# Optimization experiments

Hardware: AMD Instinct MI355X
Metric: run time of the kernel (lower is better)

Reference implementation:

```python
import jax, jax.numpy as jnp
import numpy as np

ALPHA = 0.2          # LeakyReLU negative slope
NEG_BIG = -9e15      # mask value from original code


def setup_inputs() -> dict:
    key = jax.random.key(0)
    k1, k2, k3, k4 = jax.random.split(key, 4)
    B, N, F_in, F_out = 16, 1024, 256, 256
    x = jax.random.normal(k1, (B, N, F_in), dtype=jnp.float32)
    adj = jax.random.randint(k2, (B, N, N), 0, 2, dtype=jnp.int32)
    # xavier-uniform-like scales
    W = jax.random.normal(k3, (F_in, F_out), dtype=jnp.float32) * np.sqrt(2.0 / (F_in + F_out))
    a = jax.random.normal(k4, (2 * F_out, 1), dtype=jnp.float32) * np.sqrt(2.0 / (2 * F_out + 1))
    return {"x": x, "adj": adj, "W": W, "a": a}


def reference(x, adj, W, a):
    # x: [B,N,Fin], adj: [B,N,N] (int mask), W: [Fin,Fout], a: [2*Fout,1]
    F_out = a.shape[0] // 2
    h = jnp.einsum("bni,io->bno", x, W)            # [B,N,Fout]
    # Decompose a into left/right halves: e_ij = lrelu(a_l.h_i + a_r.h_j)
    a_l = a[:F_out, 0]                               # [Fout]
    a_r = a[F_out:, 0]                               # [Fout]
    el = h @ a_l                                     # [B,N] score contribution of target i
    er = h @ a_r                                     # [B,N] score contribution of source j
    e = jax.nn.leaky_relu(el[:, :, None] + er[:, None, :], ALPHA)  # [B,N,N]
    e = jnp.where(adj > 0, e, NEG_BIG)
    attn = jax.nn.softmax(e, axis=-1)                # masked softmax over neighbors j
    # weighted sum of neighbor features; concat with n_heads=1 is identity
    return jnp.einsum("bij,bjo->bio", attn, h)       # [B,N,Fout]
```

## Files before the change

kernel.cpp:

```cpp
#include <hip/hip_runtime.h>
#include <stdint.h>

#define ALPHA 0.2f
#define NEG_BIG -9000000000000000.0f
#define L2E 1.4426950408889634f

typedef __attribute__((ext_vector_type(8))) short bf16x8;
typedef __attribute__((ext_vector_type(8))) unsigned short u16x8;
typedef __attribute__((ext_vector_type(4))) float f32x4;

__device__ __forceinline__ unsigned short f2bf(float f) {
    unsigned int u = __float_as_uint(f);
    u += 0x7fffu + ((u >> 16) & 1u);
    return (unsigned short)(u >> 16);
}

__device__ __forceinline__ void gload_lds16(const void* g, void* l) {
    __builtin_amdgcn_global_load_lds(
        (const __attribute__((address_space(1))) unsigned int*)g,
        (__attribute__((address_space(3))) unsigned int*)l, 16, 0, 0);
}

__global__ void wt_wa_kernel(const float* __restrict__ W,
                             const float* __restrict__ a,
                             unsigned short* __restrict__ Wtbf,
                             float* __restrict__ wa) {
    const int t = threadIdx.x;
    if (blockIdx.x < 256) {
        const int o = blockIdx.x;
        Wtbf[o * 256 + t] = f2bf(W[t * 256 + o]);
    } else {
        float sl = 0.f, sr = 0.f;
        const float* wr = W + t * 256;
        for (int o = 0; o < 256; ++o) {
            const float wv = wr[o];
            sl += wv * a[o];
            sr += wv * a[256 + o];
        }
        wa[t] = sl;
        wa[256 + t] = sr;
    }
}

__global__ __launch_bounds__(256) void eler2x_kernel(
    const float* __restrict__ x, const float* __restrict__ wa,
    float* __restrict__ el, float* __restrict__ er,
    unsigned short* __restrict__ xbf)
{
    const int w = threadIdx.x >> 6, l = threadIdx.x & 63;
    const int r = blockIdx.x * 4 + w;
    const float4 xv = *(const float4*)(x + (size_t)r * 256 + l * 4);
    const float4 al = *(const float4*)(wa + l * 4);
    const float4 ar = *(const float4*)(wa + 256 + l * 4);

    ushort4 xb;
    xb.x = f2bf(xv.x); xb.y = f2bf(xv.y); xb.z = f2bf(xv.z); xb.w = f2bf(xv.w);
    *(ushort4*)(xbf + (size_t)r * 256 + l * 4) = xb;

    float sl = xv.x * al.x + xv.y * al.y + xv.z * al.z + xv.w * al.w;
    float sr = xv.x * ar.x + xv.y * ar.y + xv.z * ar.z + xv.w * ar.w;
#pragma unroll
    for (int off = 32; off >= 1; off >>= 1) {
        sl += __shfl_xor(sl, off);
        sr += __shfl_xor(sr, off);
    }
    if (l == 0) { el[r] = sl * L2E; er[r] = sr * L2E; }
}

__global__ __launch_bounds__(256) void gemm_h(
    const unsigned short* __restrict__ A,
    const unsigned short* __restrict__ Bt,
    unsigned short* __restrict__ C)
{
    __shared__ __align__(16) unsigned short As[2 * 64 * 64];
    __shared__ __align__(16) unsigned short Bs[2 * 128 * 64];

    const int tid = threadIdx.x;
    const int w = tid >> 6, l = tid & 63;
    const int q = l >> 4, ml = l & 15;
    const int wm = (w >> 1) * 32;
    const int wn = (w & 1) * 64;
    const int m0 = blockIdx.y * 64;
    const int n0 = blockIdx.x * 128;

    f32x4 acc[2][4];
#pragma unroll
    for (int i = 0; i < 2; ++i)
#pragma unroll
        for (int j = 0; j < 4; ++j) {
            f32x4 z = {0.f, 0.f, 0.f, 0.f};
            acc[i][j] = z;
        }

#define GSTAGE(BI, K0) do {                                                   \
    _Pragma("unroll")                                                         \
    for (int c_ = 0; c_ < 2; ++c_) {                                          \
        const int cb_ = c_ * 256 + (w << 6);                                  \
        const int p_ = cb_ + l;                                               \
        const int r_ = p_ >> 3;                                               \
        const int cc_ = (p_ & 7) ^ (r_ & 7);                                  \
        gload_lds16(A + (size_t)(m0 + r_) * 256 + (K0) + cc_ * 8,             \
                    As + (BI) * 4096 + cb_ * 8);                              \
    }                                                                         \
    _Pragma("unroll")                                                         \
    for (int c_ = 0; c_ < 4; ++c_) {                                          \
        const int cb_ = c_ * 256 + (w << 6);                                  \
        const int p_ = cb_ + l;                                               \
        const int r_ = p_ >> 3;                                               \
        const int cc_ = (p_ & 7) ^ (r_ & 7);                                  \
        gload_lds16(Bt + (size_t)(n0 + r_) * 256 + (K0) + cc_ * 8,            \
                    Bs + (BI) * 8192 + cb_ * 8);                              \
    } } while (0)

    GSTAGE(0, 0);

    for (int s = 0; s < 4; ++s) {
        const int cur = s & 1;
        if (s + 1 < 4) {
            GSTAGE((s + 1) & 1, (s + 1) * 64);
            asm volatile("s_waitcnt vmcnt(6) lgkmcnt(0)" ::: "memory");
        } else {
            asm volatile("s_waitcnt vmcnt(0) lgkmcnt(0)" ::: "memory");
        }
        __builtin_amdgcn_s_barrier();
        __builtin_amdgcn_sched_barrier(0);

        const unsigned short* Ab = As + cur * 4096;
        const unsigned short* Bb = Bs + cur * 8192;
        bf16x8 aF[2][2], bF[2][4];
#pragma unroll
        for (int ks = 0; ks < 2; ++ks) {
#pragma unroll
            for (int mt = 0; mt < 2; ++mt) {
                const int mm = wm + mt * 16 + ml;
                aF[ks][mt] = *(const bf16x8*)(Ab + (mm * 8 + ((ks * 4 + q) ^ (mm & 7))) * 8);
            }
#pragma unroll
            for (int nt = 0; nt < 4; ++nt) {
                const int nn = wn + nt * 16 + ml;
                bF[ks][nt] = *(const bf16x8*)(Bb + (nn * 8 + ((ks * 4 + q) ^ (nn & 7))) * 8);
            }
        }
#pragma unroll
        for (int ks = 0; ks < 2; ++ks)
            for (int mt = 0; mt < 2; ++mt)
                for (int nt = 0; nt < 4; ++nt)
                    acc[mt][nt] = __builtin_amdgcn_mfma_f32_16x16x32_bf16(
                        aF[ks][mt], bF[ks][nt], acc[mt][nt], 0, 0, 0);

        asm volatile("s_waitcnt lgkmcnt(0)" ::: "memory");
        __builtin_amdgcn_s_barrier();
    }
#undef GSTAGE

    for (int mt = 0; mt < 2; ++mt)
        for (int nt = 0; nt < 4; ++nt) {
            const int gn = n0 + wn + nt * 16 + ml;
            for (int r = 0; r < 4; ++r) {
                const int gm = m0 + wm + mt * 16 + q * 4 + r;
                C[(size_t)gm * 16384 + gn] = f2bf(acc[mt][nt][r]);
            }
        }
}

__global__ __launch_bounds__(512) void maskpv_kernel(
    const int* __restrict__ adj,
    const float* __restrict__ el2,
    const float* __restrict__ er2,
    const unsigned short* __restrict__ hT,
    float* __restrict__ out)
{
    __shared__ float er_s[1024];
    __shared__ float c_s[32];
    __shared__ __align__(16) unsigned short Hs[2 * 256 * 64];
    __shared__ __align__(16) unsigned short Ps[2 * 32 * 72];

    const int tid = threadIdx.x;
    const int w = tid >> 6, l = tid & 63;
    const int q = l >> 4, ml = l & 15;
    const int wm = (w >> 2) * 16;
    const int wn = (w & 3) * 64;

    const int bid = blockIdx.x;
    const int slot = bid >> 3;
    const int b = ((bid & 7) << 1) | (slot >> 5);
    const int i0 = (slot & 31) * 32;

    const int ib = tid >> 4;
    const int js = (tid & 15) * 4;
    const int rg = (b << 10) + i0 + ib;
    const float el2i = el2[rg];

    const unsigned short* hb = hT + (size_t)b * 1024;

#define STAGE(BI, T) do {                                                     \
    const int jb_ = (T) * 64;                                                 \
    _Pragma("unroll")                                                         \
    for (int c_ = 0; c_ < 4; ++c_) {                                          \
        const int cb_ = c_ * 512 + tid;                                       \
        const int r_ = cb_ >> 3;                                              \
        const int cc_ = (cb_ & 7) ^ (r_ & 7);                                 \
        gload_lds16(hb + (size_t)r_ * 16384 + jb_ + cc_ * 8,                  \
                    Hs + (BI) * 16384 + (cb_ << 3));                          \
    } } while (0)

    STAGE(0, 0);

    *(float2*)(er_s + tid * 2) = *(const float2*)(er2 + (b << 10) + tid * 2);
    asm volatile("s_waitcnt lgkmcnt(0)" ::: "memory");
    __builtin_amdgcn_s_barrier();

    unsigned mw0 = 0, mw1 = 0;
    float m1 = -3.0e38f;
    const int* arow = adj + (size_t)rg * 1024 + js;
#pragma unroll
    for (int k = 0; k < 16; ++k) {
        const int4 av = *(const int4*)(arow + k * 64);
        const float4 erv = *(const float4*)(er_s + k * 64 + js);
        float e0 = el2i + erv.x; e0 = fmaxf(e0, ALPHA * e0);
        float e1 = el2i + erv.y; e1 = fmaxf(e1, ALPHA * e1);
        float e2 = el2i + erv.z; e2 = fmaxf(e2, ALPHA * e2);
        float e3 = el2i + erv.w; e3 = fmaxf(e3, ALPHA * e3);
        const unsigned bits = (av.x > 0 ? 1u : 0u) | (av.y > 0 ? 2u : 0u) |
                              (av.z > 0 ? 4u : 0u) | (av.w > 0 ? 8u : 0u);
        e0 = av.x > 0 ? e0 : -3.0e38f;
        e1 = av.y > 0 ? e1 : -3.0e38f;
        e2 = av.z > 0 ? e2 : -3.0e38f;
        e3 = av.w > 0 ? e3 : -3.0e38f;
        m1 = fmaxf(m1, fmaxf(fmaxf(e0, e1), fmaxf(e2, e3)));
        if (k < 8) mw0 |= bits << (k * 4); else mw1 |= bits << ((k - 8) * 4);
    }
#pragma unroll
    for (int off = 1; off <= 8; off <<= 1) m1 = fmaxf(m1, __shfl_xor(m1, off));

    float s0 = 0.f, s1 = 0.f, s2 = 0.f, s3 = 0.f;
#pragma unroll
    for (int k = 0; k < 16; ++k) {
        const float4 erv = *(const float4*)(er_s + k * 64 + js);
        const unsigned mv = ((k < 8) ? (mw0 >> (k * 4)) : (mw1 >> ((k - 8) * 4))) & 0xFu;
        float e0 = el2i + erv.x; e0 = fmaxf(e0, ALPHA * e0);
        float e1 = el2i + erv.y; e1 = fmaxf(e1, ALPHA * e1);
        float e2 = el2i + erv.z; e2 = fmaxf(e2, ALPHA * e2);
        float e3 = el2i + erv.w; e3 = fmaxf(e3, ALPHA * e3);
        s0 += (mv & 1u) ? exp2f(e0 - m1) : 0.f;
        s1 += (mv & 2u) ? exp2f(e1 - m1) : 0.f;
        s2 += (mv & 4u) ? exp2f(e2 - m1) : 0.f;
        s3 += (mv & 8u) ? exp2f(e3 - m1) : 0.f;
    }
    float ssum = (s0 + s1) + (s2 + s3);
#pragma unroll
    for (int off = 1; off <= 8; off <<= 1) ssum += __shfl_xor(ssum, off);
    if ((tid & 15) == 0) c_s[ib] = m1 + log2f(ssum);
    asm volatile("s_waitcnt lgkmcnt(0)" ::: "memory");
    __builtin_amdgcn_s_barrier();
    const float c2i = c_s[ib];

    f32x4 acc[4];
#pragma unroll
    for (int j = 0; j < 4; ++j) {
        f32x4 z = {0.f, 0.f, 0.f, 0.f};
        acc[j] = z;
    }

#define BUILDR(BI, T) do {                                                    \
    const float4 ev_ = *(const float4*)(er_s + (T) * 64 + js);                \
    const unsigned mv_ =                                                      \
        (((T) < 8) ? (mw0 >> ((T) * 4)) : (mw1 >> (((T) - 8) * 4))) & 0xFu;   \
    float e0_ = el2i + ev_.x; e0_ = fmaxf(e0_, ALPHA * e0_);                  \
    float e1_ = el2i + ev_.y; e1_ = fmaxf(e1_, ALPHA * e1_);                  \
    float e2_ = el2i + ev_.z; e2_ = fmaxf(e2_, ALPHA * e2_);                  \
    float e3_ = el2i + ev_.w; e3_ = fmaxf(e3_, ALPHA * e3_);                  \
    ushort4 pv_;                                                              \
    pv_.x = (mv_ & 1u) ? f2bf(exp2f(e0_ - c2i)) : (unsigned short)0;          \
    pv_.y = (mv_ & 2u) ? f2bf(exp2f(e1_ - c2i)) : (unsigned short)0;          \
    pv_.z = (mv_ & 4u) ? f2bf(exp2f(e2_ - c2i)) : (unsigned short)0;          \
    pv_.w = (mv_ & 8u) ? f2bf(exp2f(e3_ - c2i)) : (unsigned short)0;          \
    *(ushort4*)(Ps + (BI) * 2304 + ib * 72 + js) = pv_;                       \
    } while (0)

#define COMPUTE(BI) do {                                                      \
    bf16x8 aF_[2], bF_[2][4];                                                 \
    _Pragma("unroll")                                                         \
    for (int ks_ = 0; ks_ < 2; ++ks_)                                         \
        aF_[ks_] = *(const bf16x8*)(Ps + (BI) * 2304 +                        \
                                    (wm + ml) * 72 + ks_ * 32 + q * 8);       \
    _Pragma("unroll")                                                         \
    for (int ks_ = 0; ks_ < 2; ++ks_)                                         \
        _Pragma("unroll")                                                     \
        for (int nt_ = 0; nt_ < 4; ++nt_) {                                   \
            const int oc_ = wn + nt_ * 16 + ml;                               \
            const int sl_ = (ks_ * 4 + q) ^ (oc_ & 7);                        \
            bF_[ks_][nt_] = *(const bf16x8*)(Hs + (BI) * 16384 +              \
                                             oc_ * 64 + sl_ * 8);             \
        }                                                                     \
    _Pragma("unroll")                                                         \
    for (int ks_ = 0; ks_ < 2; ++ks_)                                         \
        _Pragma("unroll")                                                     \
        for (int nt_ = 0; nt_ < 4; ++nt_)                                     \
            acc[nt_] = __builtin_amdgcn_mfma_f32_16x16x32_bf16(               \
                aF_[ks_], bF_[ks_][nt_], acc[nt_], 0, 0, 0);                  \
    } while (0)

#pragma unroll
    for (int t = 0; t < 16; ++t) {
        const int cur = t & 1;
        if (t + 1 < 16) STAGE((t + 1) & 1, t + 1);
        BUILDR(cur, t);
        if (t + 1 < 16)
            asm volatile("s_waitcnt vmcnt(4) lgkmcnt(0)" ::: "memory");
        else
            asm volatile("s_waitcnt vmcnt(0) lgkmcnt(0)" ::: "memory");
        __builtin_amdgcn_s_barrier();
        __builtin_amdgcn_sched_barrier(0);
        COMPUTE(cur);
        asm volatile("s_waitcnt lgkmcnt(0)" ::: "memory");
        __builtin_amdgcn_s_barrier();
    }

#undef STAGE
#undef BUILDR
#undef COMPUTE

    float* ob = out + (size_t)b * 262144;
#pragma unroll
    for (int nt = 0; nt < 4; ++nt) {
        const int gn = wn + nt * 16 + ml;
#pragma unroll
        for (int r = 0; r < 4; ++r) {
            const int gm = i0 + wm + q * 4 + r;
            ob[(size_t)gm * 256 + gn] = acc[nt][r];
        }
    }
}

extern "C" void kernel_launch(void* const* d_in, const int* in_sizes, int n_in,
                              void* d_out, int out_size, void* d_ws, size_t ws_size,
                              hipStream_t stream) {
    const float* x   = (const float*)d_in[0];
    const int*   adj = (const int*)d_in[1];
    const float* W   = (const float*)d_in[2];
    const float* a   = (const float*)d_in[3];
    float* out = (float*)d_out;

    char* ws = (char*)d_ws;
    unsigned short* Wtbf  = (unsigned short*)(ws);
    float* wa             = (float*)(ws + 131072);
    unsigned short* xbf   = (unsigned short*)(ws + 133120);
    unsigned short* h_T   = (unsigned short*)(ws + 8521728);
    float* el             = (float*)(ws + 16910336);
    float* er             = (float*)(ws + 16975872);

    wt_wa_kernel<<<dim3(257), dim3(256), 0, stream>>>(W, a, Wtbf, wa);

    eler2x_kernel<<<dim3(4096), dim3(256), 0, stream>>>(x, wa, el, er, xbf);

    gemm_h<<<dim3(128, 4), dim3(256), 0, stream>>>(Wtbf, xbf, h_T);

    maskpv_kernel<<<dim3(512), dim3(512), 0, stream>>>(adj, el, er, h_T, out);
}
```

Before: 153.5 us.

## Fuse softmax statistics into PV loop with deferred row normalization

Drops the two prepass loops over the adjacency row (row max, then sum of exps). Scores are now exponentiated in the main tiled loop without subtracting a row max. The row sum is accumulated from the same bf16-rounded probabilities fed to the MFMA, and the output is divided by that sum at the end. Adjacency loads are now prefetched one tile ahead inside the pipelined loop, which removes a full serial pass of loads and exps before the matrix work. The cost is numerical safety: skipping max subtraction can overflow for large scores, and a row with no neighbours would divide by zero.

Result: slower. 157.8 us (+2.8%).

```diff
diff --git a/kernel.cpp b/kernel.cpp
--- a/kernel.cpp
+++ b/kernel.cpp
@@ -171,7 +171,7 @@
     float* __restrict__ out)
 {
     __shared__ float er_s[1024];
-    __shared__ float c_s[32];
+    __shared__ float s_s[32];
     __shared__ __align__(16) unsigned short Hs[2 * 256 * 64];
     __shared__ __align__(16) unsigned short Ps[2 * 32 * 72];
 
@@ -207,53 +207,12 @@
     STAGE(0, 0);
 
     *(float2*)(er_s + tid * 2) = *(const float2*)(er2 + (b << 10) + tid * 2);
+
+    const int* arow = adj + (size_t)rg * 1024 + js;
+    int4 a_cur = *(const int4*)(arow);
+
     asm volatile("s_waitcnt lgkmcnt(0)" ::: "memory");
     __builtin_amdgcn_s_barrier();
-
-    unsigned mw0 = 0, mw1 = 0;
-    float m1 = -3.0e38f;
-    const int* arow = adj + (size_t)rg * 1024 + js;
-#pragma unroll
-    for (int k = 0; k < 16; ++k) {
-        const int4 av = *(const int4*)(arow + k * 64);
-        const float4 erv = *(const float4*)(er_s + k * 64 + js);
-        float e0 = el2i + erv.x; e0 = fmaxf(e0, ALPHA * e0);
-        float e1 = el2i + erv.y; e1 = fmaxf(e1, ALPHA * e1);
-        float e2 = el2i + erv.z; e2 = fmaxf(e2, ALPHA * e2);
-        float e3 = el2i + erv.w; e3 = fmaxf(e3, ALPHA * e3);
-        const unsigned bits = (av.x > 0 ? 1u : 0u) | (av.y > 0 ? 2u : 0u) |
-                              (av.z > 0 ? 4u : 0u) | (av.w > 0 ? 8u : 0u);
-        e0 = av.x > 0 ? e0 : -3.0e38f;
-        e1 = av.y > 0 ? e1 : -3.0e38f;
-        e2 = av.z > 0 ? e2 : -3.0e38f;
-        e3 = av.w > 0 ? e3 : -3.0e38f;
-        m1 = fmaxf(m1, fmaxf(fmaxf(e0, e1), fmaxf(e2, e3)));
-        if (k < 8) mw0 |= bits << (k * 4); else mw1 |= bits << ((k - 8) * 4);
-    }
-#pragma unroll
-    for (int off = 1; off <= 8; off <<= 1) m1 = fmaxf(m1, __shfl_xor(m1, off));
-
-    float s0 = 0.f, s1 = 0.f, s2 = 0.f, s3 = 0.f;
-#pragma unroll
-    for (int k = 0; k < 16; ++k) {
-        const float4 erv = *(const float4*)(er_s + k * 64 + js);
-        const unsigned mv = ((k < 8) ? (mw0 >> (k * 4)) : (mw1 >> ((k - 8) * 4))) & 0xFu;
-        float e0 = el2i + erv.x; e0 = fmaxf(e0, ALPHA * e0);
-        float e1 = el2i + erv.y; e1 = fmaxf(e1, ALPHA * e1);
-        float e2 = el2i + erv.z; e2 = fmaxf(e2, ALPHA * e2);
-        float e3 = el2i + erv.w; e3 = fmaxf(e3, ALPHA * e3);
-        s0 += (mv & 1u) ? exp2f(e0 - m1) : 0.f;
-        s1 += (mv & 2u) ? exp2f(e1 - m1) : 0.f;
-        s2 += (mv & 4u) ? exp2f(e2 - m1) : 0.f;
-        s3 += (mv & 8u) ? exp2f(e3 - m1) : 0.f;
-    }
-    float ssum = (s0 + s1) + (s2 + s3);
-#pragma unroll
-    for (int off = 1; off <= 8; off <<= 1) ssum += __shfl_xor(ssum, off);
-    if ((tid & 15) == 0) c_s[ib] = m1 + log2f(ssum);
-    asm volatile("s_waitcnt lgkmcnt(0)" ::: "memory");
-    __builtin_amdgcn_s_barrier();
-    const float c2i = c_s[ib];
 
     f32x4 acc[4];
 #pragma unroll
@@ -261,20 +220,23 @@
         f32x4 z = {0.f, 0.f, 0.f, 0.f};
         acc[j] = z;
     }
+    float s0 = 0.f, s1 = 0.f, s2 = 0.f, s3 = 0.f;
 
 #define BUILDR(BI, T) do {                                                    \
     const float4 ev_ = *(const float4*)(er_s + (T) * 64 + js);                \
-    const unsigned mv_ =                                                      \
-        (((T) < 8) ? (mw0 >> ((T) * 4)) : (mw1 >> (((T) - 8) * 4))) & 0xFu;   \
     float e0_ = el2i + ev_.x; e0_ = fmaxf(e0_, ALPHA * e0_);                  \
     float e1_ = el2i + ev_.y; e1_ = fmaxf(e1_, ALPHA * e1_);                  \
     float e2_ = el2i + ev_.z; e2_ = fmaxf(e2_, ALPHA * e2_);                  \
     float e3_ = el2i + ev_.w; e3_ = fmaxf(e3_, ALPHA * e3_);                  \
     ushort4 pv_;                                                              \
-    pv_.x = (mv_ & 1u) ? f2bf(exp2f(e0_ - c2i)) : (unsigned short)0;          \
-    pv_.y = (mv_ & 2u) ? f2bf(exp2f(e1_ - c2i)) : (unsigned short)0;          \
-    pv_.z = (mv_ & 4u) ? f2bf(exp2f(e2_ - c2i)) : (unsigned short)0;          \
-    pv_.w = (mv_ & 8u) ? f2bf(exp2f(e3_ - c2i)) : (unsigned short)0;          \
+    pv_.x = (a_cur.x > 0) ? f2bf(exp2f(e0_)) : (unsigned short)0;             \
+    pv_.y = (a_cur.y > 0) ? f2bf(exp2f(e1_)) : (unsigned short)0;             \
+    pv_.z = (a_cur.z > 0) ? f2bf(exp2f(e2_)) : (unsigned short)0;             \
+    pv_.w = (a_cur.w > 0) ? f2bf(exp2f(e3_)) : (unsigned short)0;             \
+    s0 += __uint_as_float((unsigned)pv_.x << 16);                             \
+    s1 += __uint_as_float((unsigned)pv_.y << 16);                             \
+    s2 += __uint_as_float((unsigned)pv_.z << 16);                             \
+    s3 += __uint_as_float((unsigned)pv_.w << 16);                             \
     *(ushort4*)(Ps + (BI) * 2304 + ib * 72 + js) = pv_;                       \
     } while (0)
 
@@ -304,8 +266,13 @@
 #pragma unroll
     for (int t = 0; t < 16; ++t) {
         const int cur = t & 1;
-        if (t + 1 < 16) STAGE((t + 1) & 1, t + 1);
+        int4 a_nxt;
+        if (t + 1 < 16) {
+            a_nxt = *(const int4*)(arow + (t + 1) * 64);
+            STAGE((t + 1) & 1, t + 1);
+        }
         BUILDR(cur, t);
+        a_cur = a_nxt;
         if (t + 1 < 16)
             asm volatile("s_waitcnt vmcnt(4) lgkmcnt(0)" ::: "memory");
         else
@@ -321,14 +288,23 @@
 #undef BUILDR
 #undef COMPUTE
 
+    float ssum = (s0 + s1) + (s2 + s3);
+#pragma unroll
+    for (int off = 1; off <= 8; off <<= 1) ssum += __shfl_xor(ssum, off);
+    if ((tid & 15) == 0) s_s[ib] = ssum;
+    __syncthreads();
+
     float* ob = out + (size_t)b * 262144;
+    float rinv[4];
+#pragma unroll
+    for (int r = 0; r < 4; ++r) rinv[r] = 1.0f / s_s[wm + q * 4 + r];
 #pragma unroll
     for (int nt = 0; nt < 4; ++nt) {
         const int gn = wn + nt * 16 + ml;
 #pragma unroll
         for (int r = 0; r < 4; ++r) {
             const int gm = i0 + wm + q * 4 + r;
-            ob[(size_t)gm * 256 + gn] = acc[nt][r];
+            ob[(size_t)gm * 256 + gn] = acc[nt][r] * rinv[r];
         }
     }
 }
```

## Split fused masked-softmax PV kernel into P-build pass and bf16 GEMM

Applied to the files above, without the earlier changes.

Replaces the fused mask/softmax/PV kernel with two kernels. The first writes unnormalized exp scores as a bf16 P matrix plus per-row denominators. The second runs a pipelined MFMA GEMM of P with h and scales the output rows by the inverse denominators. This moves the exp and mask work out of the GEMM inner loop, at the cost of a 32MB bf16 round-trip through global memory and an extra launch. The new path is taken only when the workspace is large enough, otherwise the old kernel runs.

Result: slower. 160.1 us (+4.3%).

```diff
diff --git a/kernel.cpp b/kernel.cpp
--- a/kernel.cpp
+++ b/kernel.cpp
@@ -2,11 +2,9 @@
 #include <stdint.h>
 
 #define ALPHA 0.2f
-#define NEG_BIG -9000000000000000.0f
 #define L2E 1.4426950408889634f
 
 typedef __attribute__((ext_vector_type(8))) short bf16x8;
-typedef __attribute__((ext_vector_type(8))) unsigned short u16x8;
 typedef __attribute__((ext_vector_type(4))) float f32x4;
 
 __device__ __forceinline__ unsigned short f2bf(float f) {
@@ -133,7 +131,7 @@
 #pragma unroll
             for (int mt = 0; mt < 2; ++mt) {
                 const int mm = wm + mt * 16 + ml;
-                aF[ks][mt] = *(const bf16x8*)(Ab + (mm * 8 + ((ks * 4 + q) ^ (mm & 7))) * 8);
+                aF[ks][mt] = *(const bf16x8*)(As + cur * 4096 + (mm * 8 + ((ks * 4 + q) ^ (mm & 7))) * 8);
             }
 #pragma unroll
             for (int nt = 0; nt < 4; ++nt) {
@@ -161,6 +159,163 @@
                 C[(size_t)gm * 16384 + gn] = f2bf(acc[mt][nt][r]);
             }
         }
+}
+
+__global__ __launch_bounds__(256) void pbuild_kernel(
+    const int* __restrict__ adj,
+    const float* __restrict__ el2,
+    const float* __restrict__ er2,
+    unsigned short* __restrict__ P,
+    float* __restrict__ s)
+{
+    const int w = threadIdx.x >> 6, l = threadIdx.x & 63;
+    const int row = blockIdx.x * 4 + w;
+    const int b = row >> 10;
+    const int* arow = adj + (size_t)row * 1024;
+    const float* erb = er2 + (b << 10);
+    const float el2i = el2[row];
+
+    float sden = 0.f;
+#pragma unroll
+    for (int it = 0; it < 4; ++it) {
+        const int j = it * 256 + l * 4;
+        const int4 av = *(const int4*)(arow + j);
+        const float4 erv = *(const float4*)(erb + j);
+        float e0 = el2i + erv.x; e0 = fmaxf(e0, ALPHA * e0);
+        float e1 = el2i + erv.y; e1 = fmaxf(e1, ALPHA * e1);
+        float e2 = el2i + erv.z; e2 = fmaxf(e2, ALPHA * e2);
+        float e3 = el2i + erv.w; e3 = fmaxf(e3, ALPHA * e3);
+        ushort4 pv;
+        pv.x = (av.x > 0) ? f2bf(exp2f(e0)) : (unsigned short)0;
+        pv.y = (av.y > 0) ? f2bf(exp2f(e1)) : (unsigned short)0;
+        pv.z = (av.z > 0) ? f2bf(exp2f(e2)) : (unsigned short)0;
+        pv.w = (av.w > 0) ? f2bf(exp2f(e3)) : (unsigned short)0;
+        sden += __uint_as_float((unsigned)pv.x << 16);
+        sden += __uint_as_float((unsigned)pv.y << 16);
+        sden += __uint_as_float((unsigned)pv.z << 16);
+        sden += __uint_as_float((unsigned)pv.w << 16);
+        *(ushort4*)(P + (size_t)row * 1024 + j) = pv;
+    }
+#pragma unroll
+    for (int off = 32; off >= 1; off >>= 1) sden += __shfl_xor(sden, off);
+    if (l == 0) s[row] = sden;
+}
+
+__global__ __launch_bounds__(256) void pvgemm_kernel(
+    const unsigned short* __restrict__ P,
+    const unsigned short* __restrict__ hT,
+    const float* __restrict__ s,
+    float* __restrict__ out)
+{
+    __shared__ __align__(16) unsigned short As[2 * 64 * 64];
+    __shared__ __align__(16) unsigned short Bs[2 * 128 * 64];
+
+    const int tid = threadIdx.x;
+    const int w = tid >> 6, l = tid & 63;
+    const int q = l >> 4, ml = l & 15;
+    const int wm = (w >> 1) * 32;
+    const int wn = (w & 1) * 64;
+
+    const int bid = blockIdx.x;
+    const int slot = bid >> 3;
+    const int b = ((bid & 7) << 1) | (slot >> 5);
+    const int rem = slot & 31;
+    const int n0 = (rem & 1) * 128;
+    const int m0 = (rem >> 1) * 64;
+
+    const unsigned short* A = P + ((size_t)b << 20);
+    const unsigned short* Bt = hT + ((size_t)b << 10);
+
+    f32x4 acc[2][4];
+#pragma unroll
+    for (int i = 0; i < 2; ++i)
+#pragma unroll
+        for (int j = 0; j < 4; ++j) {
+            f32x4 z = {0.f, 0.f, 0.f, 0.f};
+            acc[i][j] = z;
+        }
+
+#define GSTAGE(BI, K0) do {                                                   \
+    _Pragma("unroll")                                                         \
+    for (int c_ = 0; c_ < 2; ++c_) {                                          \
+        const int cb_ = c_ * 256 + (w << 6);                                  \
+        const int p_ = cb_ + l;                                               \
+        const int r_ = p_ >> 3;                                               \
+        const int cc_ = (p_ & 7) ^ (r_ & 7);                                  \
+        gload_lds16(A + (size_t)(m0 + r_) * 1024 + (K0) + cc_ * 8,            \
+                    As + (BI) * 4096 + cb_ * 8);                              \
+    }                                                                         \
+    _Pragma("unroll")                                                         \
+    for (int c_ = 0; c_ < 4; ++c_) {                                          \
+        const int cb_ = c_ * 256 + (w << 6);                                  \
+        const int p_ = cb_ + l;                                               \
+        const int r_ = p_ >> 3;                                               \
+        const int cc_ = (p_ & 7) ^ (r_ & 7);                                  \
+        gload_lds16(Bt + (size_t)(n0 + r_) * 16384 + (K0) + cc_ * 8,          \
+                    Bs + (BI) * 8192 + cb_ * 8);                              \
+    } } while (0)
+
+    GSTAGE(0, 0);
+
+    for (int ks0 = 0; ks0 < 16; ++ks0) {
+        const int cur = ks0 & 1;
+        if (ks0 + 1 < 16) {
+            GSTAGE((ks0 + 1) & 1, (ks0 + 1) * 64);
+            asm volatile("s_waitcnt vmcnt(6) lgkmcnt(0)" ::: "memory");
+        } else {
+            asm volatile("s_waitcnt vmcnt(0) lgkmcnt(0)" ::: "memory");
+        }
+        __builtin_amdgcn_s_barrier();
+        __builtin_amdgcn_sched_barrier(0);
+
+        const unsigned short* Ab = As + cur * 4096;
+        const unsigned short* Bb = Bs + cur * 8192;
+        bf16x8 aF[2][2], bF[2][4];
+#pragma unroll
+        for (int ks = 0; ks < 2; ++ks) {
+#pragma unroll
+            for (int mt = 0; mt < 2; ++mt) {
+                const int mm = wm + mt * 16 + ml;
+                aF[ks][mt] = *(const bf16x8*)(Ab + (mm * 8 + ((ks * 4 + q) ^ (mm & 7))) * 8);
+            }
+#pragma unroll
+            for (int nt = 0; nt < 4; ++nt) {
+                const int nn = wn + nt * 16 + ml;
+                bF[ks][nt] = *(const bf16x8*)(Bb + (nn * 8 + ((ks * 4 + q) ^ (nn & 7))) * 8);
+            }
+        }
+        __builtin_amdgcn_s_setprio(1);
+#pragma unroll
+        for (int ks = 0; ks < 2; ++ks)
+            for (int mt = 0; mt < 2; ++mt)
+                for (int nt = 0; nt < 4; ++nt)
+                    acc[mt][nt] = __builtin_amdgcn_mfma_f32_16x16x32_bf16(
+                        aF[ks][mt], bF[ks][nt], acc[mt][nt], 0, 0, 0);
+        __builtin_amdgcn_s_setprio(0);
+
+        asm volatile("s_waitcnt lgkmcnt(0)" ::: "memory");
+        __builtin_amdgcn_s_barrier();
+    }
+#undef GSTAGE
+
+    float* ob = out + (size_t)b * 262144;
+    const float* sb = s + (b << 10);
+#pragma unroll
+    for (int mt = 0; mt < 2; ++mt) {
+        float rinv[4];
+#pragma unroll
+        for (int r = 0; r < 4; ++r)
+            rinv[r] = 1.0f / sb[m0 + wm + mt * 16 + q * 4 + r];
+#pragma unroll
+        for (int nt = 0; nt < 4; ++nt) {
+            const int gn = n0 + wn + nt * 16 + ml;
+#pragma unroll
+            for (int r = 0; r < 4; ++r) {
+                const int gm = m0 + wm + mt * 16 + q * 4 + r;
+                ob[(size_t)gm * 256 + gn] = acc[mt][nt][r] * rinv[r];
+            }
+        }
+    }
 }
 
 __global__ __launch_bounds__(512) void maskpv_kernel(
@@ -349,6 +504,8 @@
     unsigned short* h_T   = (unsigned short*)(ws + 8521728);
     float* el             = (float*)(ws + 16910336);
     float* er             = (float*)(ws + 16975872);
+    unsigned short* P     = (unsigned short*)(ws + 17041408);
+    float* sden           = (float*)(ws + 50595840);
 
     wt_wa_kernel<<<dim3(257), dim3(256), 0, stream>>>(W, a, Wtbf, wa);
 
@@ -356,5 +513,10 @@
 
     gemm_h<<<dim3(128, 4), dim3(256), 0, stream>>>(Wtbf, xbf, h_T);
 
-    maskpv_kernel<<<dim3(512), dim3(512), 0, stream>>>(adj, el, er, h_T, out);
-}
+    if (ws_size >= (size_t)50661376) {
+        pbuild_kernel<<<dim3(4096), dim3(256), 0, stream>>>(adj, el, er, P, sden);
+        pvgemm_kernel<<<dim3(512), dim3(256), 0, stream>>>(P, h_T, sden, out);
+    } else {
+        maskpv_kernel<<<dim3(512), dim3(512), 0, stream>>>(adj, el, er, h_T, out);
+    }
+}
```
